# Kernel tuning notes

Measured on AMD Instinct MI355X. Metric: run time of the kernel, lower is better.

## Reference

```python
import jax, jax.numpy as jnp
import numpy as np

TEMPERATURE = 0.5

def setup_inputs() -> dict:
    key = jax.random.key(0)
    k1, k2 = jax.random.split(key)
    B, D = 4096, 256
    embeddings_i = jax.random.normal(k1, (B, D), dtype=jnp.float32)
    embeddings_j = jax.random.normal(k2, (B, D), dtype=jnp.float32)
    return {"embeddings_i": embeddings_i, "embeddings_j": embeddings_j}

def reference(embeddings_i, embeddings_j):
    B = embeddings_i.shape[0]
    N = 2 * B
    # concat and L2-normalize rows
    z = jnp.concatenate([embeddings_i, embeddings_j], axis=0)  # [2B, D]
    z = z / jnp.linalg.norm(z, axis=1, keepdims=True)
    # pairwise cosine similarity / temperature: [2B, 2B]
    sim = jnp.matmul(z, z.T) / TEMPERATURE
    # mask self-similarity on the diagonal with -inf
    diag = jnp.arange(N)
    sim = sim.at[diag, diag].set(-jnp.inf)
    # positive pair index for each row: i<->i+B
    labels = jnp.concatenate([jnp.arange(B, N), jnp.arange(B)], axis=0)
    # softmax cross-entropy (mean over rows)
    logp = jax.nn.log_softmax(sim, axis=1)
    loss = -jnp.mean(jnp.take_along_axis(logp, labels[:, None], axis=1))
    return loss
```

## Files before the change

### kernel.cpp

```cpp
#include <hip/hip_runtime.h>
#include <hip/hip_bf16.h>

#define N_TOT 8192
#define BHALF 4096
#define DIM   256
#define INV_T 2.0f

typedef __attribute__((ext_vector_type(8))) short bf16x8;
typedef __attribute__((ext_vector_type(4))) float f32x4;

__device__ __forceinline__ float b2f(unsigned short u) {
  union { unsigned u; float f; } cv; cv.u = ((unsigned)u) << 16; return cv.f;
}
__device__ __forceinline__ unsigned short f2b(float f) {
  union { float f; unsigned u; } cv; cv.f = f;
  unsigned u = cv.u;
  u += 0x7FFFu + ((u >> 16) & 1u);
  return (unsigned short)(u >> 16);
}

__global__ __launch_bounds__(256) void normalize_kernel(
    const float* __restrict__ ei, const float* __restrict__ ej,
    unsigned short* __restrict__ zn, float* __restrict__ S) {
  if (threadIdx.x < 4) S[blockIdx.x * 4 + threadIdx.x] = 0.f;
  const int wave = threadIdx.x >> 6, lane = threadIdx.x & 63;
  const int row = blockIdx.x * 4 + wave;
  const float* src = (row < BHALF) ? (ei + (size_t)row * DIM)
                                   : (ej + (size_t)(row - BHALF) * DIM);
  float4 v = *reinterpret_cast<const float4*>(src + lane * 4);
  float ss = v.x * v.x + v.y * v.y + v.z * v.z + v.w * v.w;
#pragma unroll
  for (int off = 32; off; off >>= 1) ss += __shfl_xor(ss, off, 64);
  float inv = rsqrtf(ss);
  ushort4 o;
  o.x = f2b(v.x * inv); o.y = f2b(v.y * inv);
  o.z = f2b(v.z * inv); o.w = f2b(v.w * inv);
  *reinterpret_cast<ushort4*>(zn + (size_t)row * DIM + lane * 4) = o;
}

__global__ __launch_bounds__(256) void simexp_kernel(
    const unsigned short* __restrict__ zn, float* __restrict__ S,
    float* __restrict__ p) {
  __shared__ __align__(16) unsigned short As[128 * 64];
  __shared__ __align__(16) unsigned short Bs[128 * 64];
  const int tid = threadIdx.x;
  const int wave = tid >> 6, lane = tid & 63;

  int t = blockIdx.x;
  int a = 0;
  while ((a + 1) * 64 - ((a + 1) * a) / 2 <= t) ++a;
  const int b = a + (t - (a * 64 - (a * (a - 1)) / 2));
  const bool offdiag = (b != a);
  const bool need_p = (b == a + 32);

  const int wr = wave >> 1, wc = wave & 1;

  f32x4 acc[4][4] = {};

  const int fragrow_a = wr * 64 + (lane & 15);
  const int fragrow_b = wc * 64 + (lane & 15);
  const int kcolb = (lane >> 4) * 16;

  const unsigned short* gA = zn + (size_t)a * 128 * DIM;
  const unsigned short* gB = zn + (size_t)b * 128 * DIM;

  const int lrow  = lane >> 3;
  const int lslot = (lane & 7) * 16;

  for (int kt = 0; kt < 4; ++kt) {
#pragma unroll
    for (int r = 0; r < 4; ++r) {
      const int c = wave * 4 + r;
      const int row = c * 8 + lrow;
      const int colb = lslot ^ ((row & 7) << 4);
      const unsigned short* sA = gA + (size_t)row * DIM + kt * 64 + (colb >> 1);
      const unsigned short* sB = gB + (size_t)row * DIM + kt * 64 + (colb >> 1);
      __builtin_amdgcn_global_load_lds(
          (const __attribute__((address_space(1))) void*)sA,
          (__attribute__((address_space(3))) void*)(As + c * 512), 16, 0, 0);
      __builtin_amdgcn_global_load_lds(
          (const __attribute__((address_space(1))) void*)sB,
          (__attribute__((address_space(3))) void*)(Bs + c * 512), 16, 0, 0);
    }
    __syncthreads();

#pragma unroll
    for (int ks = 0; ks < 2; ++ks) {
      bf16x8 af[4], bfr[4];
#pragma unroll
      for (int m = 0; m < 4; ++m) {
        const int row = fragrow_a + m * 16;
        const int byt = row * 128 + ((ks * 64 + kcolb) ^ ((row & 7) << 4));
        af[m] = *reinterpret_cast<const bf16x8*>(
            reinterpret_cast<const char*>(As) + byt);
      }
#pragma unroll
      for (int n = 0; n < 4; ++n) {
        const int row = fragrow_b + n * 16;
        const int byt = row * 128 + ((ks * 64 + kcolb) ^ ((row & 7) << 4));
        bfr[n] = *reinterpret_cast<const bf16x8*>(
            reinterpret_cast<const char*>(Bs) + byt);
      }
#pragma unroll
      for (int m = 0; m < 4; ++m)
#pragma unroll
        for (int n = 0; n < 4; ++n)
          acc[m][n] = __builtin_amdgcn_mfma_f32_16x16x32_bf16(
              af[m], bfr[n], acc[m][n], 0, 0, 0);
    }
    __syncthreads();
  }

  const int grow0 = a * 128 + wr * 64 + (lane >> 4) * 4;
  const int gcol0 = b * 128 + wc * 64 + (lane & 15);

#pragma unroll
  for (int m = 0; m < 4; ++m)
#pragma unroll
    for (int n = 0; n < 4; ++n)
#pragma unroll
      for (int r = 0; r < 4; ++r) {
        const int gr = grow0 + m * 16 + r;
        const int gc = gcol0 + n * 16;
        const float raw = acc[m][n][r];
        if (need_p && gc == gr + BHALF) p[gr] = raw * INV_T;
        float v = __expf(raw * INV_T);
        if (gr == gc) v = 0.f;
        acc[m][n][r] = v;
      }

#pragma unroll
  for (int m = 0; m < 4; ++m) {
    float rs[4];
#pragma unroll
    for (int r = 0; r < 4; ++r)
      rs[r] = acc[m][0][r] + acc[m][1][r] + acc[m][2][r] + acc[m][3][r];
#pragma unroll
    for (int off = 1; off < 16; off <<= 1) {
#pragma unroll
      for (int r = 0; r < 4; ++r) rs[r] += __shfl_xor(rs[r], off, 64);
    }
    if ((lane & 15) == 0) {
#pragma unroll
      for (int r = 0; r < 4; ++r)
        atomicAdd(&S[grow0 + m * 16 + r], rs[r]);
    }
  }

  if (offdiag) {
#pragma unroll
    for (int n = 0; n < 4; ++n) {
      float cs = 0.f;
#pragma unroll
      for (int m = 0; m < 4; ++m)
#pragma unroll
        for (int r = 0; r < 4; ++r) cs += acc[m][n][r];
      cs += __shfl_xor(cs, 16, 64);
      cs += __shfl_xor(cs, 32, 64);
      if (lane < 16) atomicAdd(&S[gcol0 + n * 16], cs);
    }
  }
}

__global__ __launch_bounds__(256) void finalize_kernel(
    const float* __restrict__ S, const float* __restrict__ p,
    float* __restrict__ out) {
  float acc = 0.f;
  for (int i = threadIdx.x; i < N_TOT; i += 256) {
    const int pi = (i < BHALF) ? i : (i - BHALF);
    acc += logf(S[i]) - p[pi];
  }
#pragma unroll
  for (int off = 32; off; off >>= 1) acc += __shfl_xor(acc, off, 64);
  __shared__ float red[4];
  const int wave = threadIdx.x >> 6, lane = threadIdx.x & 63;
  if (lane == 0) red[wave] = acc;
  __syncthreads();
  if (threadIdx.x == 0)
    out[0] = (red[0] + red[1] + red[2] + red[3]) / (float)N_TOT;
}

extern "C" void kernel_launch(void* const* d_in, const int* in_sizes, int n_in,
                              void* d_out, int out_size, void* d_ws, size_t ws_size,
                              hipStream_t stream) {
  const float* ei = (const float*)d_in[0];
  const float* ej = (const float*)d_in[1];
  float* out = (float*)d_out;

  char* ws = (char*)d_ws;
  unsigned short* zn = (unsigned short*)ws;
  float* S = (float*)(ws + (size_t)N_TOT * DIM * 2);
  float* p = (float*)(ws + (size_t)N_TOT * DIM * 2 + N_TOT * 4);

  normalize_kernel<<<N_TOT / 4, 256, 0, stream>>>(ei, ej, zn, S);
  simexp_kernel<<<(64 * 65) / 2, 256, 0, stream>>>(zn, S, p);
  finalize_kernel<<<1, 256, 0, stream>>>(S, p, out);
}
```

Before: 119.9 us.

## Double-buffer LDS tiles and fuse finalize into last simexp block

Double-buffers the shared-memory K tiles so the global-to-LDS load for the next K step is issued before computing the current one. It also removes the separate finalize launch: a global counter, reset in the normalize kernel, lets the last finishing tile block compute the log-sum loss. Loads and stores of S and p now go through atomics for visibility. This doubles LDS use per block, which may reduce occupancy, and serializes the final reduction onto one block's tail.

Measured after the change: 228.3 us. 90.5% more time.

```diff
diff --git a/kernel.cpp b/kernel.cpp
--- a/kernel.cpp
+++ b/kernel.cpp
@@ -5,6 +5,7 @@
 #define BHALF 4096
 #define DIM   256
 #define INV_T 2.0f
+#define NTILES 2080
 
 typedef __attribute__((ext_vector_type(8))) short bf16x8;
 typedef __attribute__((ext_vector_type(4))) float f32x4;
@@ -21,8 +22,10 @@
 
 __global__ __launch_bounds__(256) void normalize_kernel(
     const float* __restrict__ ei, const float* __restrict__ ej,
-    unsigned short* __restrict__ zn, float* __restrict__ S) {
+    unsigned short* __restrict__ zn, float* __restrict__ S,
+    unsigned* __restrict__ counter) {
   if (threadIdx.x < 4) S[blockIdx.x * 4 + threadIdx.x] = 0.f;
+  if (blockIdx.x == 0 && threadIdx.x == 0) *counter = 0u;
   const int wave = threadIdx.x >> 6, lane = threadIdx.x & 63;
   const int row = blockIdx.x * 4 + wave;
   const float* src = (row < BHALF) ? (ei + (size_t)row * DIM)
@@ -40,9 +43,13 @@
 
 __global__ __launch_bounds__(256) void simexp_kernel(
     const unsigned short* __restrict__ zn, float* __restrict__ S,
-    float* __restrict__ p) {
-  __shared__ __align__(16) unsigned short As[128 * 64];
-  __shared__ __align__(16) unsigned short Bs[128 * 64];
+    float* __restrict__ p, unsigned* __restrict__ counter,
+    float* __restrict__ out) {
+  __shared__ __align__(16) unsigned short As[2][128 * 64];
+  __shared__ __align__(16) unsigned short Bs[2][128 * 64];
+  __shared__ float red[4];
+  __shared__ bool lastFlag;
+
   const int tid = threadIdx.x;
   const int wave = tid >> 6, lane = tid & 63;
 
@@ -67,22 +74,29 @@
   const int lrow  = lane >> 3;
   const int lslot = (lane & 7) * 16;
 
+#define STAGE(nb, kt_) do {                                                   \
+    _Pragma("unroll")                                                         \
+    for (int r = 0; r < 4; ++r) {                                             \
+      const int c = wave * 4 + r;                                             \
+      const int row = c * 8 + lrow;                                           \
+      const int colb = lslot ^ ((row & 7) << 4);                              \
+      const unsigned short* sA = gA + (size_t)row * DIM + (kt_) * 64 + (colb >> 1); \
+      const unsigned short* sB = gB + (size_t)row * DIM + (kt_) * 64 + (colb >> 1); \
+      __builtin_amdgcn_global_load_lds(                                       \
+          (const __attribute__((address_space(1))) void*)sA,                  \
+          (__attribute__((address_space(3))) void*)(&As[nb][c * 512]), 16, 0, 0); \
+      __builtin_amdgcn_global_load_lds(                                       \
+          (const __attribute__((address_space(1))) void*)sB,                  \
+          (__attribute__((address_space(3))) void*)(&Bs[nb][c * 512]), 16, 0, 0); \
+    }                                                                         \
+  } while (0)
+
+  STAGE(0, 0);
+  __syncthreads();
+
   for (int kt = 0; kt < 4; ++kt) {
-#pragma unroll
-    for (int r = 0; r < 4; ++r) {
-      const int c = wave * 4 + r;
-      const int row = c * 8 + lrow;
-      const int colb = lslot ^ ((row & 7) << 4);
-      const unsigned short* sA = gA + (size_t)row * DIM + kt * 64 + (colb >> 1);
-      const unsigned short* sB = gB + (size_t)row * DIM + kt * 64 + (colb >> 1);
-      __builtin_amdgcn_global_load_lds(
-          (const __attribute__((address_space(1))) void*)sA,
-          (__attribute__((address_space(3))) void*)(As + c * 512), 16, 0, 0);
-      __builtin_amdgcn_global_load_lds(
-          (const __attribute__((address_space(1))) void*)sB,
-          (__attribute__((address_space(3))) void*)(Bs + c * 512), 16, 0, 0);
-    }
-    __syncthreads();
+    const int cur = kt & 1;
+    if (kt < 3) STAGE(cur ^ 1, kt + 1);
 
 #pragma unroll
     for (int ks = 0; ks < 2; ++ks) {
@@ -92,14 +106,14 @@
         const int row = fragrow_a + m * 16;
         const int byt = row * 128 + ((ks * 64 + kcolb) ^ ((row & 7) << 4));
         af[m] = *reinterpret_cast<const bf16x8*>(
-            reinterpret_cast<const char*>(As) + byt);
+            reinterpret_cast<const char*>(&As[cur][0]) + byt);
       }
 #pragma unroll
       for (int n = 0; n < 4; ++n) {
         const int row = fragrow_b + n * 16;
         const int byt = row * 128 + ((ks * 64 + kcolb) ^ ((row & 7) << 4));
         bfr[n] = *reinterpret_cast<const bf16x8*>(
-            reinterpret_cast<const char*>(Bs) + byt);
+            reinterpret_cast<const char*>(&Bs[cur][0]) + byt);
       }
 #pragma unroll
       for (int m = 0; m < 4; ++m)
@@ -110,6 +124,7 @@
     }
     __syncthreads();
   }
+#undef STAGE
 
   const int grow0 = a * 128 + wr * 64 + (lane >> 4) * 4;
   const int gcol0 = b * 128 + wc * 64 + (lane & 15);
@@ -123,7 +138,7 @@
         const int gr = grow0 + m * 16 + r;
         const int gc = gcol0 + n * 16;
         const float raw = acc[m][n][r];
-        if (need_p && gc == gr + BHALF) p[gr] = raw * INV_T;
+        if (need_p && gc == gr + BHALF) atomicExch(&p[gr], raw * INV_T);
         float v = __expf(raw * INV_T);
         if (gr == gc) v = 0.f;
         acc[m][n][r] = v;
@@ -160,24 +175,25 @@
       if (lane < 16) atomicAdd(&S[gcol0 + n * 16], cs);
     }
   }
-}
-
-__global__ __launch_bounds__(256) void finalize_kernel(
-    const float* __restrict__ S, const float* __restrict__ p,
-    float* __restrict__ out) {
-  float acc = 0.f;
-  for (int i = threadIdx.x; i < N_TOT; i += 256) {
-    const int pi = (i < BHALF) ? i : (i - BHALF);
-    acc += logf(S[i]) - p[pi];
-  }
-#pragma unroll
-  for (int off = 32; off; off >>= 1) acc += __shfl_xor(acc, off, 64);
-  __shared__ float red[4];
-  const int wave = threadIdx.x >> 6, lane = threadIdx.x & 63;
-  if (lane == 0) red[wave] = acc;
+
   __syncthreads();
-  if (threadIdx.x == 0)
-    out[0] = (red[0] + red[1] + red[2] + red[3]) / (float)N_TOT;
+  __threadfence();
+  if (tid == 0) lastFlag = (atomicAdd(counter, 1u) == NTILES - 1);
+  __syncthreads();
+  if (lastFlag) {
+    float accl = 0.f;
+    for (int i = tid; i < N_TOT; i += 256) {
+      const float Si = atomicAdd(&S[i], 0.f);
+      const float pi = atomicAdd(&p[(i < BHALF) ? i : i - BHALF], 0.f);
+      accl += logf(Si) - pi;
+    }
+#pragma unroll
+    for (int off = 32; off; off >>= 1) accl += __shfl_xor(accl, off, 64);
+    if (lane == 0) red[wave] = accl;
+    __syncthreads();
+    if (tid == 0)
+      out[0] = (red[0] + red[1] + red[2] + red[3]) / (float)N_TOT;
+  }
 }
 
 extern "C" void kernel_launch(void* const* d_in, const int* in_sizes, int n_in,
@@ -191,8 +207,8 @@
   unsigned short* zn = (unsigned short*)ws;
   float* S = (float*)(ws + (size_t)N_TOT * DIM * 2);
   float* p = (float*)(ws + (size_t)N_TOT * DIM * 2 + N_TOT * 4);
-
-  normalize_kernel<<<N_TOT / 4, 256, 0, stream>>>(ei, ej, zn, S);
-  simexp_kernel<<<(64 * 65) / 2, 256, 0, stream>>>(zn, S, p);
-  finalize_kernel<<<1, 256, 0, stream>>>(S, p, out);
-}
+  unsigned* counter = (unsigned*)(ws + (size_t)N_TOT * DIM * 2 + N_TOT * 8);
+
+  normalize_kernel<<<N_TOT / 4, 256, 0, stream>>>(ei, ej, zn, S, counter);
+  simexp_kernel<<<NTILES, 256, 0, stream>>>(zn, S, p, counter, out);
+}
```
